# Kernel optimization log

Measured on AMD Instinct MI355X. Metric: run time of the kernel, lower is better.

## Reference

```python
import jax, jax.numpy as jnp
import numpy as np

DIM, HEADS, WIN, SHIFT = 384, 12, 7, 3
H, W = 56, 56
HEAD_DIM = DIM // HEADS
SCALE = HEAD_DIM ** -0.5
N = WIN * WIN


def _relative_index():
    coords = np.stack(np.meshgrid(np.arange(WIN), np.arange(WIN), indexing='ij')).reshape(2, -1)
    rel = (coords[:, :, None] - coords[:, None, :]).transpose(1, 2, 0)
    rel[:, :, 0] += WIN - 1
    rel[:, :, 1] += WIN - 1
    rel[:, :, 0] *= 2 * WIN - 1
    return rel.sum(-1)  # [N, N] int


def _attn_mask():
    img = np.zeros((H, W), dtype=np.float32)
    cnt = 0
    sls = (slice(0, -WIN), slice(-WIN, -SHIFT), slice(-SHIFT, None))
    for hs in sls:
        for ws in sls:
            img[hs, ws] = cnt
            cnt += 1
    m = img.reshape(H // WIN, WIN, W // WIN, WIN).transpose(0, 2, 1, 3).reshape(-1, N)  # [nw, N]
    diff = m[:, None, :] - m[:, :, None]  # [nw, N, N]
    return np.where(diff != 0, -10000.0, 0.0).astype(np.float32)

REL_IDX = jnp.asarray(_relative_index())
MASK = jnp.asarray(_attn_mask())  # [nw, N, N]


def _layernorm(x, w, b):
    mu = x.mean(-1, keepdims=True)
    var = ((x - mu) ** 2).mean(-1, keepdims=True)
    return (x - mu) * jax.lax.rsqrt(var + 1e-5) * w + b


def _window_partition(x):  # [B,H,W,C] -> [B*nw, N, C]
    B, _, _, C = x.shape
    x = x.reshape(B, H // WIN, WIN, W // WIN, WIN, C)
    x = x.transpose(0, 1, 3, 2, 4, 5)
    return x.reshape(-1, N, C)


def _window_reverse(w, B):  # [B*nw, N, C] -> [B,H,W,C]
    C = w.shape[-1]
    x = w.reshape(B, H // WIN, W // WIN, WIN, WIN, C)
    x = x.transpose(0, 1, 3, 2, 4, 5)
    return x.reshape(B, H, W, C)


def setup_inputs() -> dict:
    key = jax.random.key(0)
    ks = jax.random.split(key, 12)
    s = DIM ** -0.5
    return {
        'x': jax.random.normal(ks[0], (32, H * W, DIM), jnp.float32),
        'qkv_w': jax.random.normal(ks[1], (DIM, 3 * DIM), jnp.float32) * s,  # stored [in,out]
        'qkv_b': jnp.zeros((3 * DIM,), jnp.float32),
        'proj_w': jax.random.normal(ks[2], (DIM, DIM), jnp.float32) * s,
        'proj_b': jnp.zeros((DIM,), jnp.float32),
        'rel_bias': jax.random.normal(ks[3], ((2 * WIN - 1) ** 2, HEADS), jnp.float32) * 0.02,
        'norm1_w': jnp.ones((DIM,), jnp.float32),
        'norm1_b': jnp.zeros((DIM,), jnp.float32),
        'norm2_w': jnp.ones((DIM,), jnp.float32),
        'norm2_b': jnp.zeros((DIM,), jnp.float32),
        'mlp_w1': jax.random.normal(ks[4], (DIM, 4 * DIM), jnp.float32) * s,
        'mlp_b1': jnp.zeros((4 * DIM,), jnp.float32),
        'mlp_w2': jax.random.normal(ks[5], (4 * DIM, DIM), jnp.float32) * (4 * DIM) ** -0.5,
        'mlp_b2': jnp.zeros((DIM,), jnp.float32),
    }


def _forward(x, qkv_w, qkv_b, proj_w, proj_b, rel_bias, norm1_w, norm1_b,
             norm2_w, norm2_b, mlp_w1, mlp_b1, mlp_w2, mlp_b2):
    B, L, C = x.shape
    residual = x
    h = _layernorm(x, norm1_w, norm1_b).reshape(B, H, W, C)
    h = jnp.roll(h, (-SHIFT, -SHIFT), axis=(1, 2))
    wx = _window_partition(h)  # [B_, N, C]
    B_ = wx.shape[0]

    qkv = (wx @ qkv_w + qkv_b).reshape(B_, N, 3, HEADS, HEAD_DIM)
    q, k, v = qkv[:, :, 0], qkv[:, :, 1], qkv[:, :, 2]  # [B_, N, h, d]
    attn = jnp.einsum('bnhd,bmhd->bhnm', q * SCALE, k)  # [B_, h, N, N]
    rb = rel_bias[REL_IDX.reshape(-1)].reshape(N, N, HEADS).transpose(2, 0, 1)
    attn = attn + rb[None]
    nw = MASK.shape[0]
    attn = attn.reshape(B_ // nw, nw, HEADS, N, N) + MASK[None, :, None]
    attn = jax.nn.softmax(attn.reshape(B_, HEADS, N, N), axis=-1)
    out = jnp.einsum('bhnm,bmhd->bnhd', attn, v).reshape(B_, N, C)
    out = out @ proj_w + proj_b

    h = _window_reverse(out, B)
    h = jnp.roll(h, (SHIFT, SHIFT), axis=(1, 2))
    x = h.reshape(B, L, C) + residual

    m = _layernorm(x, norm2_w, norm2_b)
    m = jax.nn.gelu(m @ mlp_w1 + mlp_b1, approximate=False) @ mlp_w2 + mlp_b2
    return x + m


def reference(x, qkv_w, qkv_b, proj_w, proj_b, rel_bias, norm1_w, norm1_b,
              norm2_w, norm2_b, mlp_w1, mlp_b1, mlp_w2, mlp_b2):
    return _forward(x, qkv_w, qkv_b, proj_w, proj_b, rel_bias, norm1_w, norm1_b,
                    norm2_w, norm2_b, mlp_w1, mlp_b1, mlp_w2, mlp_b2)
```

## Files before the change

### kernel.cpp

```cpp
#include <hip/hip_runtime.h>
#include <hip/hip_bf16.h>

typedef unsigned short u16;
typedef __bf16 bf16x8 __attribute__((ext_vector_type(8)));
typedef float f32x4 __attribute__((ext_vector_type(4)));

#define HH 56
#define WW 56
#define DIM 384
#define NTOK 100352
#define NWIN 2048
#define NN 49

__device__ __forceinline__ u16 f2bf(float f) {
    __hip_bfloat16 h = __float2bfloat16(f);
    return *reinterpret_cast<u16*>(&h);
}
__device__ __forceinline__ float bf2f(u16 u) {
    union { unsigned int i; float f; } c; c.i = ((unsigned int)u) << 16; return c.f;
}

__device__ __forceinline__ float fast_gelu(float x) {
    float au = fabsf(x) * 0.70710678118654752f;
    float t = __builtin_amdgcn_rcpf(fmaf(0.3275911f, au, 1.0f));
    float p = fmaf(t, 1.061405429f, -1.453152027f);
    p = fmaf(t, p, 1.421413741f);
    p = fmaf(t, p, -0.284496736f);
    p = fmaf(t, p, 0.254829592f);
    p = p * t;
    float e = __expf(-au * au);
    float erfau = fmaf(-p, e, 1.0f);
    float erfx = __builtin_copysignf(erfau, x);
    return 0.5f * x * (1.0f + erfx);
}

#define GLD_LDS(gp, lp) __builtin_amdgcn_global_load_lds( \
    (const __attribute__((address_space(1))) void*)(gp), \
    (__attribute__((address_space(3))) void*)(lp), 16, 0, 0)

__global__ void castT(const float* __restrict__ in, u16* __restrict__ out, int K, int N) {
    int i = blockIdx.x * 256 + threadIdx.x;
    if (i < N * K) {
        int n = i / K, kk = i - n * K;
        out[i] = f2bf(in[(size_t)kk * N + n]);
    }
}

__global__ void bias_kernel(const float* __restrict__ rel_bias, float* __restrict__ Tb) {
    int ty = blockIdx.x / 12, h = blockIdx.x - ty * 12;
    for (int i = threadIdx.x; i < 4096; i += 256) {
        int q = i >> 6, kk = i & 63;
        float v;
        if (kk >= 49) v = -1e30f;
        else if (q >= 49) v = 0.f;
        else {
            int rn = q / 7, cn = q - rn * 7;
            int rm = kk / 7, cm = kk - rm * 7;
            float rb = rel_bias[((rn - rm + 6) * 13 + (cn - cm + 6)) * 12 + h];
            int h0 = (ty >> 1) ? 49 : 0;
            int w0 = (ty & 1) ? 49 : 0;
            int hn = h0 + rn, hm = h0 + rm, wn = w0 + cn, wm = w0 + cm;
            int regn = (hn < 49 ? 0 : (hn < 53 ? 1 : 2)) * 3 + (wn < 49 ? 0 : (wn < 53 ? 1 : 2));
            int regm = (hm < 49 ? 0 : (hm < 53 ? 1 : 2)) * 3 + (wm < 49 ? 0 : (wm < 53 ? 1 : 2));
            v = rb + ((regn == regm) ? 0.f : -10000.f);
        }
        Tb[(size_t)blockIdx.x * 4096 + i] = v;
    }
}

template<bool WIN_MAP>
__global__ __launch_bounds__(256) void ln_kernel(
    const float* __restrict__ x, const float* __restrict__ w, const float* __restrict__ b,
    u16* __restrict__ out)
{
    int token = blockIdx.x * 4 + (threadIdx.x >> 6);
    int lane = threadIdx.x & 63;
    const float* row = x + (size_t)token * DIM;
    float v[6]; float sum = 0.f, sq = 0.f;
#pragma unroll
    for (int j = 0; j < 3; j++) {
        float2 p = *(const float2*)(row + lane * 2 + j * 128);
        v[2*j] = p.x; v[2*j+1] = p.y;
        sum += p.x + p.y; sq += p.x * p.x + p.y * p.y;
    }
#pragma unroll
    for (int off = 32; off; off >>= 1) { sum += __shfl_xor(sum, off); sq += __shfl_xor(sq, off); }
    float mu = sum * (1.f / DIM);
    float rstd = rsqrtf(sq * (1.f / DIM) - mu * mu + 1e-5f);
    size_t obase;
    if (WIN_MAP) {
        int b_ = token / 3136, hw = token - b_ * 3136;
        int h = hw / WW, wc_ = hw - h * WW;
        int hr = h - 3; if (hr < 0) hr += HH;
        int wr = wc_ - 3; if (wr < 0) wr += WW;
        int win = b_ * 64 + (hr / 7) * 8 + (wr / 7);
        int n = (hr % 7) * 7 + (wr % 7);
        obase = ((size_t)win * NN + n) * DIM;
    } else {
        obase = (size_t)token * DIM;
    }
#pragma unroll
    for (int j = 0; j < 3; j++) {
        int c = lane * 2 + j * 128;
        float a0 = (v[2*j]   - mu) * rstd * w[c]   + b[c];
        float a1 = (v[2*j+1] - mu) * rstd * w[c+1] + b[c+1];
        unsigned int pair = (unsigned int)f2bf(a0) | ((unsigned int)f2bf(a1) << 16);
        *(unsigned int*)(out + obase + c) = pair;
    }
}

template<int EPI>
__global__ __launch_bounds__(256) void gemm_kernel(
    const u16* __restrict__ A, const u16* __restrict__ Bt,
    const float* __restrict__ bias, const float* __restrict__ resid,
    void* __restrict__ outp, int N, int K, int BNT)
{
    __shared__ u16 sA[2][128 * 32];
    __shared__ u16 sB[2][128 * 32];
    const int tid = threadIdx.x;
    const int lane = tid & 63;
    const int wave = tid >> 6;
    const int wr = wave >> 1, wc = wave & 1;

    const int q8 = gridDim.x >> 3;
    const int wg = (blockIdx.x & 7) * q8 + (blockIdx.x >> 3);
    const int bm = wg / BNT, bn = wg - bm * BNT;

    f32x4 acc[4][4] = {};

    const u16* Arow0 = A + (size_t)(bm * 128 + (tid >> 2)) * K + (tid & 3) * 8;
    const u16* Arow1 = Arow0 + (size_t)64 * K;
    const u16* Brow0 = Bt + (size_t)(bn * 128 + (tid >> 2)) * K + (tid & 3) * 8;
    const u16* Brow1 = Brow0 + (size_t)64 * K;

    const int nt = K >> 5;

    GLD_LDS(Arow0, &sA[0][wave * 512]);
    GLD_LDS(Arow1, &sA[0][2048 + wave * 512]);
    GLD_LDS(Brow0, &sB[0][wave * 512]);
    GLD_LDS(Brow1, &sB[0][2048 + wave * 512]);
    __syncthreads();

    for (int t = 0; t < nt; t++) {
        const int cur = t & 1;
        if (t + 1 < nt) {
            int kt = (t + 1) * 32;
            GLD_LDS(Arow0 + kt, &sA[cur ^ 1][wave * 512]);
            GLD_LDS(Arow1 + kt, &sA[cur ^ 1][2048 + wave * 512]);
            GLD_LDS(Brow0 + kt, &sB[cur ^ 1][wave * 512]);
            GLD_LDS(Brow1 + kt, &sB[cur ^ 1][2048 + wave * 512]);
        }
        bf16x8 af[4], bfr[4];
#pragma unroll
        for (int m = 0; m < 4; m++)
            af[m] = *(const bf16x8*)&sA[cur][(wr * 64 + m * 16 + (lane & 15)) * 32 + (lane >> 4) * 8];
#pragma unroll
        for (int n = 0; n < 4; n++)
            bfr[n] = *(const bf16x8*)&sB[cur][(wc * 64 + n * 16 + (lane & 15)) * 32 + (lane >> 4) * 8];
#pragma unroll
        for (int m = 0; m < 4; m++)
#pragma unroll
            for (int n = 0; n < 4; n++)
                acc[m][n] = __builtin_amdgcn_mfma_f32_16x16x32_bf16(af[m], bfr[n], acc[m][n], 0, 0, 0);
        __syncthreads();
    }

    const int l15 = lane & 15;
    const int col0 = bn * 128 + wc * 64 + l15;
    float bias4[4];
#pragma unroll
    for (int nn = 0; nn < 4; nn++) bias4[nn] = bias[col0 + nn * 16];

#pragma unroll
    for (int m = 0; m < 4; m++) {
#pragma unroll
        for (int r = 0; r < 4; r++) {
            int row = bm * 128 + wr * 64 + m * 16 + ((lane >> 4) << 2) + r;
            size_t obase;
            if (EPI == 1) {
                int win = row / NN, n = row - win * NN;
                int b_ = win >> 6, wi = win & 63;
                int hr = (wi >> 3) * 7 + n / 7;
                int wcl = (wi & 7) * 7 + n % 7;
                int hf = hr + 3; if (hf >= HH) hf -= HH;
                int wf = wcl + 3; if (wf >= WW) wf -= WW;
                obase = ((size_t)b_ * 3136 + hf * WW + wf) * DIM;
            } else {
                obase = (size_t)row * N;
            }
#pragma unroll
            for (int nn = 0; nn < 4; nn++) {
                int col = col0 + nn * 16;
                float val = acc[m][nn][r] + bias4[nn];
                if (EPI == 0) {
                    ((u16*)outp)[obase + col] = f2bf(val);
                } else if (EPI == 1) {
                    ((float*)outp)[obase + col] = val + resid[obase + col];
                } else if (EPI == 2) {
                    ((u16*)outp)[obase + col] = f2bf(fast_gelu(val));
                } else {
                    ((float*)outp)[obase + col] = val + resid[obase + col];
                }
            }
        }
    }
}

__global__ __launch_bounds__(256) void attn_kernel(
    const u16* __restrict__ qkv, const float* __restrict__ Tb,
    u16* __restrict__ attn_out)
{
    __shared__ u16 smem[4][6912];
    const int win = blockIdx.x;
    const int wave = threadIdx.x >> 6;
    const int lane = threadIdx.x & 63;
    const int head = blockIdx.y * 4 + wave;
    const int l15 = lane & 15, g = lane >> 4;

    u16* Vt = smem[wave];
    u16* P  = Vt + 2304;

    const u16* qkvw = qkv + (size_t)win * NN * 1152 + head * 32;

    {
        int m = lane;
        bool real = m < NN;
        const u16* vrow = qkvw + (size_t)(real ? m : 0) * 1152 + 768;
        int4 z = {0,0,0,0};
        int4 c0 = real ? *(const int4*)(vrow)      : z;
        int4 c1 = real ? *(const int4*)(vrow + 8)  : z;
        int4 c2 = real ? *(const int4*)(vrow + 16) : z;
        int4 c3 = real ? *(const int4*)(vrow + 24) : z;
        u16 vals[32];
        *(int4*)&vals[0]  = c0; *(int4*)&vals[8]  = c1;
        *(int4*)&vals[16] = c2; *(int4*)&vals[24] = c3;
#pragma unroll
        for (int d = 0; d < 32; d++) Vt[d * 72 + m] = vals[d];
    }

    bf16x8 kf[4], qf[4];
#pragma unroll
    for (int t = 0; t < 4; t++) {
        int row = t * 16 + l15; if (row > 48) row = 48;
        const u16* base = qkvw + (size_t)row * 1152 + g * 8;
        kf[t] = *(const bf16x8*)(base + 384);
        qf[t] = *(const bf16x8*)(base);
    }
    f32x4 s[4][4];
#pragma unroll
    for (int mt = 0; mt < 4; mt++)
#pragma unroll
        for (int nt = 0; nt < 4; nt++) {
            f32x4 zero = {};
            s[mt][nt] = __builtin_amdgcn_mfma_f32_16x16x32_bf16(kf[mt], qf[nt], zero, 0, 0, 0);
        }

    const int wi = win & 63;
    const int ty = (((wi >> 3) == 7) ? 2 : 0) + (((wi & 7) == 7) ? 1 : 0);
    const float* tbb = Tb + (((size_t)ty * 12 + head) << 12);
    const float SCALE = 0.17677669529663687f;
#pragma unroll
    for (int nt = 0; nt < 4; nt++) {
        int q = nt * 16 + l15;
        const float* trow = tbb + q * 64 + g * 4;
        f32x4 b[4];
#pragma unroll
        for (int mt = 0; mt < 4; mt++) b[mt] = *(const f32x4*)(trow + mt * 16);
        float mx = -3e38f;
#pragma unroll
        for (int mt = 0; mt < 4; mt++)
#pragma unroll
            for (int r = 0; r < 4; r++) {
                float v = s[mt][nt][r] * SCALE + b[mt][r];
                s[mt][nt][r] = v;
                mx = fmaxf(mx, v);
            }
        mx = fmaxf(mx, __shfl_xor(mx, 16));
        mx = fmaxf(mx, __shfl_xor(mx, 32));
        float sum = 0.f;
#pragma unroll
        for (int mt = 0; mt < 4; mt++)
#pragma unroll
            for (int r = 0; r < 4; r++) {
                float e = __expf(s[mt][nt][r] - mx);
                s[mt][nt][r] = e;
                sum += e;
            }
        sum += __shfl_xor(sum, 16);
        sum += __shfl_xor(sum, 32);
        float inv = 1.f / sum;
#pragma unroll
        for (int mt = 0; mt < 4; mt++) {
            unsigned int p01 = (unsigned int)f2bf(s[mt][nt][0] * inv) | ((unsigned int)f2bf(s[mt][nt][1] * inv) << 16);
            unsigned int p23 = (unsigned int)f2bf(s[mt][nt][2] * inv) | ((unsigned int)f2bf(s[mt][nt][3] * inv) << 16);
            uint2 pk; pk.x = p01; pk.y = p23;
            *(uint2*)&P[(unsigned)q * 72 + mt * 16 + g * 4] = pk;
        }
    }

    bf16x8 vf[2][2];
#pragma unroll
    for (int ks = 0; ks < 2; ks++)
#pragma unroll
        for (int dt = 0; dt < 2; dt++)
            vf[ks][dt] = *(const bf16x8*)&Vt[(dt * 16 + l15) * 72 + ks * 32 + g * 8];

    f32x4 o[4][2] = {};
#pragma unroll
    for (int nt = 0; nt < 4; nt++) {
        bf16x8 pf0 = *(const bf16x8*)&P[(nt * 16 + l15) * 72 + g * 8];
        bf16x8 pf1 = *(const bf16x8*)&P[(nt * 16 + l15) * 72 + 32 + g * 8];
#pragma unroll
        for (int dt = 0; dt < 2; dt++) {
            o[nt][dt] = __builtin_amdgcn_mfma_f32_16x16x32_bf16(pf0, vf[0][dt], o[nt][dt], 0, 0, 0);
            o[nt][dt] = __builtin_amdgcn_mfma_f32_16x16x32_bf16(pf1, vf[1][dt], o[nt][dt], 0, 0, 0);
        }
    }

#pragma unroll
    for (int nt = 0; nt < 4; nt++)
#pragma unroll
        for (int r = 0; r < 4; r++) {
            int q = nt * 16 + 4 * g + r;
            if (q < NN) {
                size_t ob = ((size_t)win * NN + q) * DIM + head * 32;
                attn_out[ob + l15]      = f2bf(o[nt][0][r]);
                attn_out[ob + 16 + l15] = f2bf(o[nt][1][r]);
            }
        }
}

extern "C" void kernel_launch(void* const* d_in, const int* in_sizes, int n_in,
                              void* d_out, int out_size, void* d_ws, size_t ws_size,
                              hipStream_t stream)
{
    const float* x      = (const float*)d_in[0];
    const float* qkv_w  = (const float*)d_in[1];
    const float* qkv_b  = (const float*)d_in[2];
    const float* proj_w = (const float*)d_in[3];
    const float* proj_b = (const float*)d_in[4];
    const float* rel_b  = (const float*)d_in[5];
    const float* n1w    = (const float*)d_in[6];
    const float* n1b    = (const float*)d_in[7];
    const float* n2w    = (const float*)d_in[8];
    const float* n2b    = (const float*)d_in[9];
    const float* w1     = (const float*)d_in[10];
    const float* b1     = (const float*)d_in[11];
    const float* w2     = (const float*)d_in[12];
    const float* b2     = (const float*)d_in[13];

    char* ws = (char*)d_ws;
    u16* hidden  = (u16*)(ws);
    u16* qkvbuf  = hidden;
    float* Tb    = (float*)(ws + 231211008);
    u16* wxbuf   = (u16*)(ws + 308281344);
    u16* qkv_wt  = (u16*)(ws + 385351680);
    u16* proj_wt = (u16*)(ws + 386236416);
    u16* w1t     = (u16*)(ws + 386531328);
    u16* w2t     = (u16*)(ws + 387710976);

    castT<<<(1152*384 + 255) / 256, 256, 0, stream>>>(qkv_w, qkv_wt, 384, 1152);
    castT<<<(384*384  + 255) / 256, 256, 0, stream>>>(proj_w, proj_wt, 384, 384);
    castT<<<(384*1536 + 255) / 256, 256, 0, stream>>>(w1, w1t, 384, 1536);
    castT<<<(1536*384 + 255) / 256, 256, 0, stream>>>(w2, w2t, 1536, 384);
    bias_kernel<<<48, 256, 0, stream>>>(rel_b, Tb);

    ln_kernel<true><<<NTOK / 4, 256, 0, stream>>>(x, n1w, n1b, wxbuf);
    gemm_kernel<0><<<784 * 9, 256, 0, stream>>>(wxbuf, qkv_wt, qkv_b, nullptr, qkvbuf, 1152, 384, 9);
    attn_kernel<<<dim3(NWIN, 3), 256, 0, stream>>>(qkvbuf, Tb, wxbuf);
    gemm_kernel<1><<<784 * 3, 256, 0, stream>>>(wxbuf, proj_wt, proj_b, x, d_out, 384, 384, 3);
    ln_kernel<false><<<NTOK / 4, 256, 0, stream>>>((const float*)d_out, n2w, n2b, wxbuf);
    gemm_kernel<2><<<784 * 12, 256, 0, stream>>>(wxbuf, w1t, b1, nullptr, hidden, 1536, 384, 12);
    gemm_kernel<3><<<784 * 3, 256, 0, stream>>>(hidden, w2t, b2, (const float*)d_out, d_out, 384, 1536, 3);
}
```

Measured before the change: 944.3 us.

## Triple-buffer GEMM LDS pipeline with XOR-swizzled layout and single barrier

Measured after the change: 929.2 us. About the same (-1.6%).

```diff
diff --git a/kernel.cpp b/kernel.cpp
--- a/kernel.cpp
+++ b/kernel.cpp
@@ -110,13 +110,13 @@
 }
 
 template<int EPI>
-__global__ __launch_bounds__(256) void gemm_kernel(
+__global__ __launch_bounds__(256, 3) void gemm_kernel(
     const u16* __restrict__ A, const u16* __restrict__ Bt,
     const float* __restrict__ bias, const float* __restrict__ resid,
     void* __restrict__ outp, int N, int K, int BNT)
 {
-    __shared__ u16 sA[2][128 * 32];
-    __shared__ u16 sB[2][128 * 32];
+    __shared__ u16 sA[3][4096];
+    __shared__ u16 sB[3][4096];
     const int tid = threadIdx.x;
     const int lane = tid & 63;
     const int wave = tid >> 6;
@@ -128,44 +128,62 @@
 
     f32x4 acc[4][4] = {};
 
-    const u16* Arow0 = A + (size_t)(bm * 128 + (tid >> 2)) * K + (tid & 3) * 8;
+    const int r0 = tid >> 2;
+    const int sg = (tid & 3) ^ (r0 & 3);
+    const u16* Arow0 = A + (size_t)(bm * 128 + r0) * K + sg * 8;
     const u16* Arow1 = Arow0 + (size_t)64 * K;
-    const u16* Brow0 = Bt + (size_t)(bn * 128 + (tid >> 2)) * K + (tid & 3) * 8;
+    const u16* Brow0 = Bt + (size_t)(bn * 128 + r0) * K + sg * 8;
     const u16* Brow1 = Brow0 + (size_t)64 * K;
 
     const int nt = K >> 5;
 
-    GLD_LDS(Arow0, &sA[0][wave * 512]);
-    GLD_LDS(Arow1, &sA[0][2048 + wave * 512]);
-    GLD_LDS(Brow0, &sB[0][wave * 512]);
-    GLD_LDS(Brow1, &sB[0][2048 + wave * 512]);
-    __syncthreads();
-
+#define STAGE(t, buf) do { \
+        int kt_ = (t) * 32; \
+        GLD_LDS(Arow0 + kt_, &sA[buf][wave * 512]); \
+        GLD_LDS(Arow1 + kt_, &sA[buf][2048 + wave * 512]); \
+        GLD_LDS(Brow0 + kt_, &sB[buf][wave * 512]); \
+        GLD_LDS(Brow1 + kt_, &sB[buf][2048 + wave * 512]); \
+    } while (0)
+
+    STAGE(0, 0);
+    STAGE(1, 1);
+
+    const int l15 = lane & 15, g = lane >> 4;
+    const int ssr = (g ^ (l15 & 3)) * 8;
+
+    int buf = 0;
     for (int t = 0; t < nt; t++) {
-        const int cur = t & 1;
         if (t + 1 < nt) {
-            int kt = (t + 1) * 32;
-            GLD_LDS(Arow0 + kt, &sA[cur ^ 1][wave * 512]);
-            GLD_LDS(Arow1 + kt, &sA[cur ^ 1][2048 + wave * 512]);
-            GLD_LDS(Brow0 + kt, &sB[cur ^ 1][wave * 512]);
-            GLD_LDS(Brow1 + kt, &sB[cur ^ 1][2048 + wave * 512]);
+            asm volatile("s_waitcnt vmcnt(4)" ::: "memory");
+        } else {
+            asm volatile("s_waitcnt vmcnt(0)" ::: "memory");
+        }
+        __builtin_amdgcn_s_barrier();
+        __builtin_amdgcn_sched_barrier(0);
+        if (t + 2 < nt) {
+            int nb = buf + 2; if (nb >= 3) nb -= 3;
+            STAGE(t + 2, nb);
         }
         bf16x8 af[4], bfr[4];
 #pragma unroll
-        for (int m = 0; m < 4; m++)
-            af[m] = *(const bf16x8*)&sA[cur][(wr * 64 + m * 16 + (lane & 15)) * 32 + (lane >> 4) * 8];
-#pragma unroll
-        for (int n = 0; n < 4; n++)
-            bfr[n] = *(const bf16x8*)&sB[cur][(wc * 64 + n * 16 + (lane & 15)) * 32 + (lane >> 4) * 8];
+        for (int m = 0; m < 4; m++) {
+            int row = wr * 64 + m * 16 + l15;
+            af[m] = *(const bf16x8*)&sA[buf][row * 32 + ssr];
+        }
+#pragma unroll
+        for (int n = 0; n < 4; n++) {
+            int row = wc * 64 + n * 16 + l15;
+            bfr[n] = *(const bf16x8*)&sB[buf][row * 32 + ssr];
+        }
 #pragma unroll
         for (int m = 0; m < 4; m++)
 #pragma unroll
             for (int n = 0; n < 4; n++)
                 acc[m][n] = __builtin_amdgcn_mfma_f32_16x16x32_bf16(af[m], bfr[n], acc[m][n], 0, 0, 0);
-        __syncthreads();
-    }
-
-    const int l15 = lane & 15;
+        buf = buf + 1; if (buf >= 3) buf = 0;
+    }
+#undef STAGE
+
     const int col0 = bn * 128 + wc * 64 + l15;
     float bias4[4];
 #pragma unroll
@@ -175,7 +193,7 @@
     for (int m = 0; m < 4; m++) {
 #pragma unroll
         for (int r = 0; r < 4; r++) {
-            int row = bm * 128 + wr * 64 + m * 16 + ((lane >> 4) << 2) + r;
+            int row = bm * 128 + wr * 64 + m * 16 + (g << 2) + r;
             size_t obase;
             if (EPI == 1) {
                 int win = row / NN, n = row - win * NN;
```
